# Kernel tuning notes

Hardware: AMD Instinct MI355X
Metric: run time of the kernel (lower is better)

## Reference

```python
import jax, jax.numpy as jnp
import numpy as np

D_MODEL = 1024
N_HEADS = 16
D_K = D_MODEL // N_HEADS


def setup_inputs() -> dict:
    key = jax.random.key(0)
    ks = jax.random.split(key, 11)
    B, S = 2, 2048
    scale = 1.0 / np.sqrt(D_MODEL)
    return {
        "query": jax.random.normal(ks[0], (B, S, D_MODEL), jnp.float32),
        "key": jax.random.normal(ks[1], (B, S, D_MODEL), jnp.float32),
        "value": jax.random.normal(ks[2], (B, S, D_MODEL), jnp.float32),
        "w_q": jax.random.normal(ks[3], (D_MODEL, D_MODEL), jnp.float32) * scale,
        "b_q": jnp.zeros((D_MODEL,), jnp.float32),
        "w_k": jax.random.normal(ks[4], (D_MODEL, D_MODEL), jnp.float32) * scale,
        "b_k": jnp.zeros((D_MODEL,), jnp.float32),
        "w_v": jax.random.normal(ks[5], (D_MODEL, D_MODEL), jnp.float32) * scale,
        "b_v": jnp.zeros((D_MODEL,), jnp.float32),
        "w_o": jax.random.normal(ks[6], (D_MODEL, D_MODEL), jnp.float32) * scale,
        "b_o": jnp.zeros((D_MODEL,), jnp.float32),
    }


def reference(query, key, value, w_q, b_q, w_k, b_k, w_v, b_v, w_o, b_o):
    B, S, _ = query.shape
    # Linear projections (torch Linear: x @ W.T + b), split heads -> (B, H, S, Dk)
    def proj(x, w, b):
        y = jnp.einsum('bsd,ed->bse', x, w) + b
        return y.reshape(B, -1, N_HEADS, D_K).transpose(0, 2, 1, 3)
    q = proj(query, w_q, b_q)
    k = proj(key, w_k, b_k)
    v = proj(value, w_v, b_v)
    # Scaled dot-product attention (full O(S^2) scores, faithful to source)
    scores = jnp.einsum('bhqd,bhkd->bhqk', q, k) / np.sqrt(D_K)
    attn = jax.nn.softmax(scores, axis=-1)
    out = jnp.einsum('bhqk,bhkd->bhqd', attn, v)  # (B, H, S, Dk)
    out = out.transpose(0, 2, 1, 3).reshape(B, S, D_MODEL)
    out = jnp.einsum('bsd,ed->bse', out, w_o) + b_o
    return out
```

## Files before the change

### kernel.cpp

```cpp
#include <hip/hip_runtime.h>
#include <hip/hip_bf16.h>

#define DM 1024
#define NH 16
#define DKH 64
#define BB 2
#define SS 2048
#define MM (BB*SS)
#define HKB 1024

typedef __bf16 v8bf __attribute__((ext_vector_type(8)));
typedef float  v4f  __attribute__((ext_vector_type(4)));
typedef float  v16f __attribute__((ext_vector_type(16)));

__device__ __forceinline__ unsigned short f2bf(float f) {
    union { float f; unsigned int u; } v; v.f = f;
    unsigned int u = v.u;
    unsigned int r = (u + 0x7fffu + ((u >> 16) & 1u)) >> 16;
    return (unsigned short)r;
}

__device__ __forceinline__ int cvtpk(float lo, float hi) {
    int r;
    asm("v_cvt_pk_bf16_f32 %0, %1, %2" : "=v"(r) : "v"(lo), "v"(hi));
    return r;
}

__device__ __forceinline__ void pl32swap(int& a, int& b) {
    asm("v_permlane32_swap_b32 %0, %1" : "+v"(a), "+v"(b));
}

__device__ __forceinline__ void gl16(const unsigned short* g, unsigned short* l) {
    auto gp = reinterpret_cast<const __attribute__((address_space(1))) unsigned int*>(
        reinterpret_cast<uintptr_t>(g));
    auto lp = reinterpret_cast<__attribute__((address_space(3))) unsigned int*>(
        reinterpret_cast<uintptr_t>(l));
    __builtin_amdgcn_global_load_lds(gp, lp, 16, 0, 0);
}

__global__ __launch_bounds__(256) void cvt_to_bf16(
    const float* __restrict__ xq, const float* __restrict__ xk, const float* __restrict__ xv,
    const float* __restrict__ wq, const float* __restrict__ wk, const float* __restrict__ wv,
    const float* __restrict__ wo, unsigned short* __restrict__ dst)
{
    const int y = blockIdx.y;
    const float* src;
    size_t n, off;
    if (y < 3) {
        src = (y == 0) ? xq : (y == 1) ? xk : xv;
        n = (size_t)MM * DM;
        off = (size_t)y * MM * DM;
    } else {
        src = (y == 3) ? wq : (y == 4) ? wk : (y == 5) ? wv : wo;
        n = (size_t)DM * DM;
        off = (size_t)3 * MM * DM + (size_t)(y - 3) * DM * DM;
    }
    unsigned short* d = dst + off;
    const size_t stride = (size_t)gridDim.x * blockDim.x;
    for (size_t i = (size_t)blockIdx.x * blockDim.x + threadIdx.x; i * 8 < n; i += stride) {
        float4 a = ((const float4*)src)[2 * i];
        float4 b = ((const float4*)src)[2 * i + 1];
        uint4 o;
        o.x = (unsigned)cvtpk(a.x, a.y);
        o.y = (unsigned)cvtpk(a.z, a.w);
        o.z = (unsigned)cvtpk(b.x, b.y);
        o.w = (unsigned)cvtpk(b.z, b.w);
        ((uint4*)d)[i] = o;
    }
}

__global__ __launch_bounds__(256) void proj_qkv_b(
    const unsigned short* __restrict__ xb, const unsigned short* __restrict__ wb,
    const float* __restrict__ bq, const float* __restrict__ bk, const float* __restrict__ bv,
    unsigned short* __restrict__ q_ws, unsigned short* __restrict__ k_ws,
    unsigned short* __restrict__ vt_ws)
{
    const int z = blockIdx.z;
    const unsigned short* X = xb + (size_t)z * MM * DM;
    const unsigned short* W = wb + (size_t)z * DM * DM;
    const float* bias = (z == 0) ? bq : (z == 1) ? bk : bv;

    __shared__ unsigned short lA[3][128 * 32];
    __shared__ unsigned short lB[3][128 * 32];

    const int t = threadIdx.x;
    const int lane = t & 63, w = t >> 6;
    const int wm = w >> 1, wn = w & 1;
    const int g = lane >> 4, lr = lane & 15;

    const int hid = blockIdx.y * 8 + blockIdx.x;
    const int xcd = hid & 7, slot = hid >> 3;
    const int mbase = (xcd * 4 + (slot & 3)) * 128;
    const int nbase = (slot >> 2) * 128;

    const int srow = lane >> 2;
    const int scol = (lane & 3) * 8;

    v4f acc[4][4];
#pragma unroll
    for (int i = 0; i < 4; ++i)
#pragma unroll
        for (int j = 0; j < 4; ++j)
            acc[i][j] = (v4f){0.f, 0.f, 0.f, 0.f};

    auto stage = [&](int bi, int kb) {
        gl16(X + (size_t)(mbase + w * 16 + srow) * DM + kb + scol,      &lA[bi][w * 512]);
        gl16(X + (size_t)(mbase + 64 + w * 16 + srow) * DM + kb + scol, &lA[bi][(w + 4) * 512]);
        gl16(W + (size_t)(nbase + w * 16 + srow) * DM + kb + scol,      &lB[bi][w * 512]);
        gl16(W + (size_t)(nbase + 64 + w * 16 + srow) * DM + kb + scol, &lB[bi][(w + 4) * 512]);
    };
    auto compute = [&](int bi) {
        v8bf af[4], bf4[4];
#pragma unroll
        for (int mt = 0; mt < 4; ++mt)
            af[mt] = *(const v8bf*)(&lA[bi][(wm * 64 + mt * 16 + lr) * 32 + g * 8]);
#pragma unroll
        for (int nt = 0; nt < 4; ++nt)
            bf4[nt] = *(const v8bf*)(&lB[bi][(wn * 64 + nt * 16 + lr) * 32 + g * 8]);
#pragma unroll
        for (int mt = 0; mt < 4; ++mt)
#pragma unroll
            for (int nt = 0; nt < 4; ++nt)
                acc[mt][nt] = __builtin_amdgcn_mfma_f32_16x16x32_bf16(af[mt], bf4[nt], acc[mt][nt], 0, 0, 0);
    };

    stage(0, 0);
    stage(1, 32);
    int bcur = 0;
#pragma unroll 1
    for (int ki = 0; ki < 30; ++ki) {
        int bnext = bcur + 2; if (bnext >= 3) bnext -= 3;
        stage(bnext, (ki + 2) * 32);
        asm volatile("s_waitcnt vmcnt(8)" ::: "memory");
        __builtin_amdgcn_sched_barrier(0);
        __builtin_amdgcn_s_barrier();
        __builtin_amdgcn_sched_barrier(0);
        compute(bcur);
        __builtin_amdgcn_sched_barrier(0);
        __builtin_amdgcn_s_barrier();
        bcur = (bcur == 2) ? 0 : bcur + 1;
    }
    asm volatile("s_waitcnt vmcnt(4)" ::: "memory");
    __builtin_amdgcn_sched_barrier(0);
    __builtin_amdgcn_s_barrier();
    __builtin_amdgcn_sched_barrier(0);
    compute(bcur);
    __builtin_amdgcn_sched_barrier(0);
    __builtin_amdgcn_s_barrier();
    bcur = (bcur == 2) ? 0 : bcur + 1;
    asm volatile("s_waitcnt vmcnt(0)" ::: "memory");
    __builtin_amdgcn_sched_barrier(0);
    __builtin_amdgcn_s_barrier();
    __builtin_amdgcn_sched_barrier(0);
    compute(bcur);

    const float scale = (z == 0) ? 0.18033688011112042f : 1.0f;
#pragma unroll
    for (int nt = 0; nt < 4; ++nt) {
        int e = nbase + wn * 64 + nt * 16 + lr;
        float bval = bias[e];
        int h = e >> 6, dk = e & 63;
#pragma unroll
        for (int mt = 0; mt < 4; ++mt) {
#pragma unroll
            for (int r = 0; r < 4; ++r) {
                int m = mbase + wm * 64 + mt * 16 + g * 4 + r;
                float val = (acc[mt][nt][r] + bval) * scale;
                unsigned short o = f2bf(val);
                int b = m >> 11, s = m & 2047;
                if (z == 2) {
                    vt_ws[((size_t)(b * NH + h) * DKH + dk) * SS + s] = o;
                } else {
                    unsigned short* dst = (z == 0) ? q_ws : k_ws;
                    dst[((size_t)(b * NH + h) * SS + s) * DKH + dk] = o;
                }
            }
        }
    }
}

#define KB 64
#define LDP 72
#define TILE 4608

__global__ __launch_bounds__(512, 4) void attn_kernel(
    const unsigned short* __restrict__ q_ws, const unsigned short* __restrict__ k_ws,
    const unsigned short* __restrict__ vt_ws, unsigned short* __restrict__ o_ws)
{
    __shared__ __align__(16) unsigned short lsBuf[2 * 4 * TILE];

    const int t = threadIdx.x, l = t & 63, w = t >> 6;
    const int h = l >> 5, ql = l & 31;
    const int qg = w >> 1, hf = w & 1;

    const int hid = blockIdx.x;
    const int slot = hid >> 3;
    const int bh = (hid & 7) * 4 + (slot & 3);
    const int qp = slot >> 2;
    const int q0 = qp * 128 + qg * 32;

    const unsigned short* Kb = k_ws + (size_t)bh * SS * DKH;
    const unsigned short* Vb = vt_ws + (size_t)bh * DKH * SS;

    v8bf qf[4];
#pragma unroll
    for (int c = 0; c < 4; ++c)
        qf[c] = *(const v8bf*)(q_ws + ((size_t)bh * SS + q0 + ql) * DKH + c * 16 + h * 8);

    v16f oT[2];
#pragma unroll
    for (int d = 0; d < 2; ++d)
#pragma unroll
        for (int r = 0; r < 16; ++r) oT[d][r] = 0.f;
    float l_lane = 0.f;
    const v16f z16 = {};

    const int r0s = t >> 3, c0s = (t & 7) * 8;
    uint4 k0r, k1r, v0r, v1r;

    k0r = *(const uint4*)(Kb + (size_t)(r0s) * DKH + c0s);
    v0r = *(const uint4*)(Vb + (size_t)r0s * SS + c0s);
    k1r = *(const uint4*)(Kb + (size_t)(HKB + r0s) * DKH + c0s);
    v1r = *(const uint4*)(Vb + (size_t)r0s * SS + HKB + c0s);
    {
        unsigned short* B0 = lsBuf;
        *(uint4*)&B0[0 * TILE + r0s * LDP + c0s] = k0r;
        *(uint4*)&B0[1 * TILE + r0s * LDP + c0s] = v0r;
        *(uint4*)&B0[2 * TILE + r0s * LDP + c0s] = k1r;
        *(uint4*)&B0[3 * TILE + r0s * LDP + c0s] = v1r;
    }
    k0r = *(const uint4*)(Kb + (size_t)(KB + r0s) * DKH + c0s);
    v0r = *(const uint4*)(Vb + (size_t)r0s * SS + KB + c0s);
    k1r = *(const uint4*)(Kb + (size_t)(HKB + KB + r0s) * DKH + c0s);
    v1r = *(const uint4*)(Vb + (size_t)r0s * SS + HKB + KB + c0s);
    __syncthreads();

    const int NT = 16;
    int p = 0;
    for (int tt = 0; tt < NT; ++tt) {
        unsigned short* Kp = lsBuf + p * (4 * TILE) + hf * (2 * TILE);
        unsigned short* Vp = Kp + TILE;
        if (tt + 1 < NT) {
            unsigned short* Bn = lsBuf + (p ^ 1) * (4 * TILE);
            *(uint4*)&Bn[0 * TILE + r0s * LDP + c0s] = k0r;
            *(uint4*)&Bn[1 * TILE + r0s * LDP + c0s] = v0r;
            *(uint4*)&Bn[2 * TILE + r0s * LDP + c0s] = k1r;
            *(uint4*)&Bn[3 * TILE + r0s * LDP + c0s] = v1r;
        }
        if (tt + 2 < NT) {
            int kt2 = (tt + 2) * KB;
            k0r = *(const uint4*)(Kb + (size_t)(kt2 + r0s) * DKH + c0s);
            v0r = *(const uint4*)(Vb + (size_t)r0s * SS + kt2 + c0s);
            k1r = *(const uint4*)(Kb + (size_t)(HKB + kt2 + r0s) * DKH + c0s);
            v1r = *(const uint4*)(Vb + (size_t)r0s * SS + HKB + kt2 + c0s);
        }

        v16f sT[2];
        __builtin_amdgcn_s_setprio(1);
#pragma unroll
        for (int kb = 0; kb < 2; ++kb) {
            v8bf kf = *(const v8bf*)&Kp[(kb * 32 + ql) * LDP + h * 8];
            sT[kb] = __builtin_amdgcn_mfma_f32_32x32x16_bf16(kf, qf[0], z16, 0, 0, 0);
        }
#pragma unroll
        for (int c = 1; c < 4; ++c)
#pragma unroll
            for (int kb = 0; kb < 2; ++kb) {
                v8bf kf = *(const v8bf*)&Kp[(kb * 32 + ql) * LDP + c * 16 + h * 8];
                sT[kb] = __builtin_amdgcn_mfma_f32_32x32x16_bf16(kf, qf[c], sT[kb], 0, 0, 0);
            }
        __builtin_amdgcn_s_setprio(0);

        float rs0 = 0.f, rs1 = 0.f, rs2 = 0.f, rs3 = 0.f;
#pragma unroll
        for (int kb = 0; kb < 2; ++kb)
#pragma unroll
            for (int r = 0; r < 16; r += 4) {
                float e0 = __builtin_amdgcn_exp2f(sT[kb][r + 0]);
                float e1 = __builtin_amdgcn_exp2f(sT[kb][r + 1]);
                float e2 = __builtin_amdgcn_exp2f(sT[kb][r + 2]);
                float e3 = __builtin_amdgcn_exp2f(sT[kb][r + 3]);
                sT[kb][r + 0] = e0; sT[kb][r + 1] = e1;
                sT[kb][r + 2] = e2; sT[kb][r + 3] = e3;
                rs0 += e0; rs1 += e1; rs2 += e2; rs3 += e3;
            }
        l_lane += (rs0 + rs1) + (rs2 + rs3);

        v8bf pfrag[4];
#pragma unroll
        for (int c = 0; c < 4; ++c) {
            const int cc = c & 1, kb = c >> 1;
            int A0 = cvtpk(sT[kb][8 * cc + 0], sT[kb][8 * cc + 1]);
            int A1 = cvtpk(sT[kb][8 * cc + 2], sT[kb][8 * cc + 3]);
            int B0 = cvtpk(sT[kb][8 * cc + 4], sT[kb][8 * cc + 5]);
            int B1 = cvtpk(sT[kb][8 * cc + 6], sT[kb][8 * cc + 7]);
            pl32swap(A0, B0);
            pl32swap(A1, B1);
            union { int i[4]; v8bf v; } u;
            u.i[0] = A0; u.i[1] = A1; u.i[2] = B0; u.i[3] = B1;
            pfrag[c] = u.v;
        }

        __builtin_amdgcn_s_setprio(1);
#pragma unroll
        for (int db = 0; db < 2; ++db)
#pragma unroll
            for (int c = 0; c < 4; ++c) {
                v8bf vf = *(const v8bf*)&Vp[(db * 32 + ql) * LDP + c * 16 + h * 8];
                oT[db] = __builtin_amdgcn_mfma_f32_32x32x16_bf16(vf, pfrag[c], oT[db], 0, 0, 0);
            }
        __builtin_amdgcn_s_setprio(0);

        __syncthreads();
        p ^= 1;
    }

    float lsum = l_lane + __shfl_xor(l_lane, 32);
    float* lsf = (float*)lsBuf;
    const int row = qg * 32 + ql;
#pragma unroll
    for (int db = 0; db < 2; ++db)
#pragma unroll
        for (int r = 0; r < 16; ++r) {
            int d = db * 32 + (r & 3) + 8 * (r >> 2) + 4 * h;
            lsf[(hf * 128 + row) * 65 + d] = oT[db][r];
        }
    if (h == 0) lsf[(hf * 128 + row) * 65 + 64] = lsum;
    __syncthreads();

    const int orow = t >> 2;
    const int ck = t & 3;
    const float* e0 = lsf + orow * 65;
    const float* e1 = lsf + (128 + orow) * 65;
    const float linv = 1.0f / (e0[64] + e1[64]);
    const int b = bh >> 4, hh = bh & 15;
    const int d0 = ck * 16;
    unsigned short* op = o_ws + ((size_t)b * SS + qp * 128 + orow) * DM + hh * DKH + d0;
    uint4 o0, o1;
    o0.x = (unsigned)cvtpk((e0[d0+0]+e1[d0+0])*linv,  (e0[d0+1]+e1[d0+1])*linv);
    o0.y = (unsigned)cvtpk((e0[d0+2]+e1[d0+2])*linv,  (e0[d0+3]+e1[d0+3])*linv);
    o0.z = (unsigned)cvtpk((e0[d0+4]+e1[d0+4])*linv,  (e0[d0+5]+e1[d0+5])*linv);
    o0.w = (unsigned)cvtpk((e0[d0+6]+e1[d0+6])*linv,  (e0[d0+7]+e1[d0+7])*linv);
    o1.x = (unsigned)cvtpk((e0[d0+8]+e1[d0+8])*linv,  (e0[d0+9]+e1[d0+9])*linv);
    o1.y = (unsigned)cvtpk((e0[d0+10]+e1[d0+10])*linv,(e0[d0+11]+e1[d0+11])*linv);
    o1.z = (unsigned)cvtpk((e0[d0+12]+e1[d0+12])*linv,(e0[d0+13]+e1[d0+13])*linv);
    o1.w = (unsigned)cvtpk((e0[d0+14]+e1[d0+14])*linv,(e0[d0+15]+e1[d0+15])*linv);
    *(uint4*)op = o0;
    *(uint4*)(op + 8) = o1;
}

__global__ __launch_bounds__(256) void proj_o_b(
    const unsigned short* __restrict__ A, const unsigned short* __restrict__ W,
    const float* __restrict__ bo, float* __restrict__ out)
{
    __shared__ unsigned short lA[3][128 * 32];
    __shared__ unsigned short lB[3][64 * 32];

    const int t = threadIdx.x;
    const int lane = t & 63, w = t >> 6;
    const int wm = w >> 1, wn = w & 1;
    const int g = lane >> 4, lr = lane & 15;

    const int hid = blockIdx.y * 16 + blockIdx.x;
    const int xcd = hid & 7, slot = hid >> 3;
    const int mbase = (xcd * 4 + (slot & 3)) * 128;
    const int nbase = (slot >> 2) * 64;

    const int srow = lane >> 2;
    const int scol = (lane & 3) * 8;

    v4f acc[4][2];
#pragma unroll
    for (int i = 0; i < 4; ++i)
#pragma unroll
        for (int j = 0; j < 2; ++j)
            acc[i][j] = (v4f){0.f, 0.f, 0.f, 0.f};

    auto stage = [&](int bi, int kb) {
        gl16(A + (size_t)(mbase + w * 16 + srow) * DM + kb + scol,      &lA[bi][w * 512]);
        gl16(A + (size_t)(mbase + 64 + w * 16 + srow) * DM + kb + scol, &lA[bi][(w + 4) * 512]);
        gl16(W + (size_t)(nbase + w * 16 + srow) * DM + kb + scol,      &lB[bi][w * 512]);
    };
    auto compute = [&](int bi) {
        v8bf af[4], bf4[2];
#pragma unroll
        for (int mt = 0; mt < 4; ++mt)
            af[mt] = *(const v8bf*)(&lA[bi][(wm * 64 + mt * 16 + lr) * 32 + g * 8]);
#pragma unroll
        for (int nt = 0; nt < 2; ++nt)
            bf4[nt] = *(const v8bf*)(&lB[bi][(wn * 32 + nt * 16 + lr) * 32 + g * 8]);
#pragma unroll
        for (int mt = 0; mt < 4; ++mt)
#pragma unroll
            for (int nt = 0; nt < 2; ++nt)
                acc[mt][nt] = __builtin_amdgcn_mfma_f32_16x16x32_bf16(af[mt], bf4[nt], acc[mt][nt], 0, 0, 0);
    };

    stage(0, 0);
    stage(1, 32);
    int bcur = 0;
#pragma unroll 1
    for (int ki = 0; ki < 30; ++ki) {
        int bnext = bcur + 2; if (bnext >= 3) bnext -= 3;
        stage(bnext, (ki + 2) * 32);
        asm volatile("s_waitcnt vmcnt(6)" ::: "memory");
        __builtin_amdgcn_sched_barrier(0);
        __builtin_amdgcn_s_barrier();
        __builtin_amdgcn_sched_barrier(0);
        compute(bcur);
        __builtin_amdgcn_sched_barrier(0);
        __builtin_amdgcn_s_barrier();
        bcur = (bcur == 2) ? 0 : bcur + 1;
    }
    asm volatile("s_waitcnt vmcnt(3)" ::: "memory");
    __builtin_amdgcn_sched_barrier(0);
    __builtin_amdgcn_s_barrier();
    __builtin_amdgcn_sched_barrier(0);
    compute(bcur);
    __builtin_amdgcn_sched_barrier(0);
    __builtin_amdgcn_s_barrier();
    bcur = (bcur == 2) ? 0 : bcur + 1;
    asm volatile("s_waitcnt vmcnt(0)" ::: "memory");
    __builtin_amdgcn_sched_barrier(0);
    __builtin_amdgcn_s_barrier();
    __builtin_amdgcn_sched_barrier(0);
    compute(bcur);

#pragma unroll
    for (int nt = 0; nt < 2; ++nt) {
        int e = nbase + wn * 32 + nt * 16 + lr;
        float bval = bo[e];
#pragma unroll
        for (int mt = 0; mt < 4; ++mt) {
#pragma unroll
            for (int r = 0; r < 4; ++r) {
                int m = mbase + wm * 64 + mt * 16 + g * 4 + r;
                out[(size_t)m * DM + e] = acc[mt][nt][r] + bval;
            }
        }
    }
}

extern "C" void kernel_launch(void* const* d_in, const int* in_sizes, int n_in,
                              void* d_out, int out_size, void* d_ws, size_t ws_size,
                              hipStream_t stream) {
    const float* q  = (const float*)d_in[0];
    const float* k  = (const float*)d_in[1];
    const float* v  = (const float*)d_in[2];
    const float* wq = (const float*)d_in[3];
    const float* bq = (const float*)d_in[4];
    const float* wk = (const float*)d_in[5];
    const float* bk = (const float*)d_in[6];
    const float* wv = (const float*)d_in[7];
    const float* bv = (const float*)d_in[8];
    const float* wo = (const float*)d_in[9];
    const float* bo = (const float*)d_in[10];
    float* out = (float*)d_out;

    unsigned short* ws    = (unsigned short*)d_ws;
    unsigned short* q_ws  = ws;
    unsigned short* k_ws  = q_ws + (size_t)MM * DM;
    unsigned short* vt_ws = k_ws + (size_t)MM * DM;
    unsigned short* xb    = vt_ws + (size_t)MM * DM;
    unsigned short* wb    = xb + (size_t)3 * MM * DM;
    unsigned short* o_ws  = xb;

    cvt_to_bf16<<<dim3(256, 7), 256, 0, stream>>>(q, k, v, wq, wk, wv, wo, xb);
    proj_qkv_b<<<dim3(8, 32, 3), 256, 0, stream>>>(xb, wb, bq, bk, bv, q_ws, k_ws, vt_ws);
    attn_kernel<<<dim3(512), 512, 0, stream>>>(q_ws, k_ws, vt_ws, o_ws);
    proj_o_b<<<dim3(16, 32), 256, 0, stream>>>(o_ws, wb + (size_t)3 * DM * DM, bo, out);
}
```

Measured before the change: 120.4 us.

## Fuse fp32-to-bf16 activation conversion into QKV projection GEMM loads

The activations are no longer converted to bf16 by a separate pass. The QKV projection kernel now loads fp32 activations into registers, converts them and writes them to a double-buffered LDS tile, while the weights stay on the async global-to-LDS path. The standalone conversion kernel now handles only the weights, which removes one full write and re-read of the activation tensors. The attention kernel also swaps __syncthreads for an lgkmcnt wait plus raw barrier, and interleaves exp/pack with the PV MFMAs per key block. In exchange the A tile goes through registers, which adds VGPR pressure and makes the prefetch less asynchronous.

Result: faster. 117.3 us (-2.5%).

```diff
diff --git a/kernel.cpp b/kernel.cpp
--- a/kernel.cpp
+++ b/kernel.cpp
@@ -38,24 +38,14 @@
     __builtin_amdgcn_global_load_lds(gp, lp, 16, 0, 0);
 }
 
-__global__ __launch_bounds__(256) void cvt_to_bf16(
-    const float* __restrict__ xq, const float* __restrict__ xk, const float* __restrict__ xv,
+__global__ __launch_bounds__(256) void cvt_w(
     const float* __restrict__ wq, const float* __restrict__ wk, const float* __restrict__ wv,
     const float* __restrict__ wo, unsigned short* __restrict__ dst)
 {
     const int y = blockIdx.y;
-    const float* src;
-    size_t n, off;
-    if (y < 3) {
-        src = (y == 0) ? xq : (y == 1) ? xk : xv;
-        n = (size_t)MM * DM;
-        off = (size_t)y * MM * DM;
-    } else {
-        src = (y == 3) ? wq : (y == 4) ? wk : (y == 5) ? wv : wo;
-        n = (size_t)DM * DM;
-        off = (size_t)3 * MM * DM + (size_t)(y - 3) * DM * DM;
-    }
-    unsigned short* d = dst + off;
+    const float* src = (y == 0) ? wq : (y == 1) ? wk : (y == 2) ? wv : wo;
+    unsigned short* d = dst + (size_t)y * DM * DM;
+    const size_t n = (size_t)DM * DM;
     const size_t stride = (size_t)gridDim.x * blockDim.x;
     for (size_t i = (size_t)blockIdx.x * blockDim.x + threadIdx.x; i * 8 < n; i += stride) {
         float4 a = ((const float4*)src)[2 * i];
@@ -70,17 +60,18 @@
 }
 
 __global__ __launch_bounds__(256) void proj_qkv_b(
-    const unsigned short* __restrict__ xb, const unsigned short* __restrict__ wb,
+    const float* __restrict__ Xq, const float* __restrict__ Xk, const float* __restrict__ Xv,
+    const unsigned short* __restrict__ wb,
     const float* __restrict__ bq, const float* __restrict__ bk, const float* __restrict__ bv,
     unsigned short* __restrict__ q_ws, unsigned short* __restrict__ k_ws,
     unsigned short* __restrict__ vt_ws)
 {
     const int z = blockIdx.z;
-    const unsigned short* X = xb + (size_t)z * MM * DM;
+    const float* X = (z == 0) ? Xq : (z == 1) ? Xk : Xv;
     const unsigned short* W = wb + (size_t)z * DM * DM;
     const float* bias = (z == 0) ? bq : (z == 1) ? bk : bv;
 
-    __shared__ unsigned short lA[3][128 * 32];
+    __shared__ unsigned short lA[2][128 * 32];
     __shared__ unsigned short lB[3][128 * 32];
 
     const int t = threadIdx.x;
@@ -95,6 +86,8 @@
 
     const int srow = lane >> 2;
     const int scol = (lane & 3) * 8;
+    const int arow = t >> 1;
+    const int acg  = (t & 1) * 16;
 
     v4f acc[4][4];
 #pragma unroll
@@ -103,20 +96,32 @@
         for (int j = 0; j < 4; ++j)
             acc[i][j] = (v4f){0.f, 0.f, 0.f, 0.f};
 
-    auto stage = [&](int bi, int kb) {
-        gl16(X + (size_t)(mbase + w * 16 + srow) * DM + kb + scol,      &lA[bi][w * 512]);
-        gl16(X + (size_t)(mbase + 64 + w * 16 + srow) * DM + kb + scol, &lA[bi][(w + 4) * 512]);
+    float4 ar0, ar1, ar2, ar3;
+    auto loadA = [&](int kb) {
+        const float4* p = (const float4*)(X + (size_t)(mbase + arow) * DM + kb + acg);
+        ar0 = p[0]; ar1 = p[1]; ar2 = p[2]; ar3 = p[3];
+    };
+    auto writeA = [&](int bi) {
+        uint4 o0, o1;
+        o0.x = (unsigned)cvtpk(ar0.x, ar0.y); o0.y = (unsigned)cvtpk(ar0.z, ar0.w);
+        o0.z = (unsigned)cvtpk(ar1.x, ar1.y); o0.w = (unsigned)cvtpk(ar1.z, ar1.w);
+        o1.x = (unsigned)cvtpk(ar2.x, ar2.y); o1.y = (unsigned)cvtpk(ar2.z, ar2.w);
+        o1.z = (unsigned)cvtpk(ar3.x, ar3.y); o1.w = (unsigned)cvtpk(ar3.z, ar3.w);
+        *(uint4*)&lA[bi][arow * 32 + acg]     = o0;
+        *(uint4*)&lA[bi][arow * 32 + acg + 8] = o1;
+    };
+    auto stageB = [&](int bi, int kb) {
         gl16(W + (size_t)(nbase + w * 16 + srow) * DM + kb + scol,      &lB[bi][w * 512]);
         gl16(W + (size_t)(nbase + 64 + w * 16 + srow) * DM + kb + scol, &lB[bi][(w + 4) * 512]);
     };
-    auto compute = [&](int bi) {
+    auto compute = [&](const unsigned short* A_, const unsigned short* B_) {
         v8bf af[4], bf4[4];
 #pragma unroll
         for (int mt = 0; mt < 4; ++mt)
-            af[mt] = *(const v8bf*)(&lA[bi][(wm * 64 + mt * 16 + lr) * 32 + g * 8]);
+            af[mt] = *(const v8bf*)(&A_[(wm * 64 + mt * 16 + lr) * 32 + g * 8]);
 #pragma unroll
         for (int nt = 0; nt < 4; ++nt)
-            bf4[nt] = *(const v8bf*)(&lB[bi][(wn * 64 + nt * 16 + lr) * 32 + g * 8]);
+            bf4[nt] = *(const v8bf*)(&B_[(wn * 64 + nt * 16 + lr) * 32 + g * 8]);
 #pragma unroll
         for (int mt = 0; mt < 4; ++mt)
 #pragma unroll
@@ -124,35 +129,30 @@
                 acc[mt][nt] = __builtin_amdgcn_mfma_f32_16x16x32_bf16(af[mt], bf4[nt], acc[mt][nt], 0, 0, 0);
     };
 
-    stage(0, 0);
-    stage(1, 32);
-    int bcur = 0;
+    loadA(0);
+    stageB(0, 0);
+    writeA(0);
+    loadA(32);
+    stageB(1, 32);
+
 #pragma unroll 1
-    for (int ki = 0; ki < 30; ++ki) {
-        int bnext = bcur + 2; if (bnext >= 3) bnext -= 3;
-        stage(bnext, (ki + 2) * 32);
-        asm volatile("s_waitcnt vmcnt(8)" ::: "memory");
+    for (int ki = 0; ki < 31; ++ki) {
+        writeA((ki + 1) & 1);
+        if (ki < 30) {
+            loadA((ki + 2) * 32);
+            stageB((ki + 2) % 3, (ki + 2) * 32);
+            asm volatile("s_waitcnt vmcnt(6) lgkmcnt(0)" ::: "memory");
+        } else {
+            asm volatile("s_waitcnt vmcnt(0) lgkmcnt(0)" ::: "memory");
+        }
         __builtin_amdgcn_sched_barrier(0);
         __builtin_amdgcn_s_barrier();
         __builtin_amdgcn_sched_barrier(0);
-        compute(bcur);
+        compute(lA[ki & 1], lB[ki % 3]);
         __builtin_amdgcn_sched_barrier(0);
         __builtin_amdgcn_s_barrier();
-        bcur = (bcur == 2) ? 0 : bcur + 1;
-    }
-    asm volatile("s_waitcnt vmcnt(4)" ::: "memory");
-    __builtin_amdgcn_sched_barrier(0);
-    __builtin_amdgcn_s_barrier();
-    __builtin_amdgcn_sched_barrier(0);
-    compute(bcur);
-    __builtin_amdgcn_sched_barrier(0);
-    __builtin_amdgcn_s_barrier();
-    bcur = (bcur == 2) ? 0 : bcur + 1;
-    asm volatile("s_waitcnt vmcnt(0)" ::: "memory");
-    __builtin_amdgcn_sched_barrier(0);
-    __builtin_amdgcn_s_barrier();
-    __builtin_amdgcn_sched_barrier(0);
-    compute(bcur);
+    }
+    compute(lA[31 & 1], lB[31 % 3]);
 
     const float scale = (z == 0) ? 0.18033688011112042f : 1.0f;
 #pragma unroll
@@ -233,7 +233,10 @@
     v0r = *(const uint4*)(Vb + (size_t)r0s * SS + KB + c0s);
     k1r = *(const uint4*)(Kb + (size_t)(HKB + KB + r0s) * DKH + c0s);
     v1r = *(const uint4*)(Vb + (size_t)r0s * SS + HKB + KB + c0s);
-    __syncthreads();
+    asm volatile("s_waitcnt lgkmcnt(0)" ::: "memory");
+    __builtin_amdgcn_sched_barrier(0);
+    __builtin_amdgcn_s_barrier();
+    __builtin_amdgcn_sched_barrier(0);
 
     const int NT = 16;
     int p = 0;
@@ -271,9 +274,10 @@
             }
         __builtin_amdgcn_s_setprio(0);
 
-        float rs0 = 0.f, rs1 = 0.f, rs2 = 0.f, rs3 = 0.f;
-#pragma unroll
-        for (int kb = 0; kb < 2; ++kb)
+        v8bf pfrag[4];
+#pragma unroll
+        for (int kb = 0; kb < 2; ++kb) {
+            float rs0 = 0.f, rs1 = 0.f, rs2 = 0.f, rs3 = 0.f;
 #pragma unroll
             for (int r = 0; r < 16; r += 4) {
                 float e0 = __builtin_amdgcn_exp2f(sT[kb][r + 0]);
@@ -284,34 +288,37 @@
                 sT[kb][r + 2] = e2; sT[kb][r + 3] = e3;
                 rs0 += e0; rs1 += e1; rs2 += e2; rs3 += e3;
             }
-        l_lane += (rs0 + rs1) + (rs2 + rs3);
-
-        v8bf pfrag[4];
-#pragma unroll
-        for (int c = 0; c < 4; ++c) {
-            const int cc = c & 1, kb = c >> 1;
-            int A0 = cvtpk(sT[kb][8 * cc + 0], sT[kb][8 * cc + 1]);
-            int A1 = cvtpk(sT[kb][8 * cc + 2], sT[kb][8 * cc + 3]);
-            int B0 = cvtpk(sT[kb][8 * cc + 4], sT[kb][8 * cc + 5]);
-            int B1 = cvtpk(sT[kb][8 * cc + 6], sT[kb][8 * cc + 7]);
-            pl32swap(A0, B0);
-            pl32swap(A1, B1);
-            union { int i[4]; v8bf v; } u;
-            u.i[0] = A0; u.i[1] = A1; u.i[2] = B0; u.i[3] = B1;
-            pfrag[c] = u.v;
-        }
-
-        __builtin_amdgcn_s_setprio(1);
-#pragma unroll
-        for (int db = 0; db < 2; ++db)
-#pragma unroll
-            for (int c = 0; c < 4; ++c) {
-                v8bf vf = *(const v8bf*)&Vp[(db * 32 + ql) * LDP + c * 16 + h * 8];
-                oT[db] = __builtin_amdgcn_mfma_f32_32x32x16_bf16(vf, pfrag[c], oT[db], 0, 0, 0);
+            l_lane += (rs0 + rs1) + (rs2 + rs3);
+
+#pragma unroll
+            for (int cc = 0; cc < 2; ++cc) {
+                int A0 = cvtpk(sT[kb][8 * cc + 0], sT[kb][8 * cc + 1]);
+                int A1 = cvtpk(sT[kb][8 * cc + 2], sT[kb][8 * cc + 3]);
+                int B0 = cvtpk(sT[kb][8 * cc + 4], sT[kb][8 * cc + 5]);
+                int B1 = cvtpk(sT[kb][8 * cc + 6], sT[kb][8 * cc + 7]);
+                pl32swap(A0, B0);
+                pl32swap(A1, B1);
+                union { int i[4]; v8bf v; } u;
+                u.i[0] = A0; u.i[1] = A1; u.i[2] = B0; u.i[3] = B1;
+                pfrag[kb * 2 + cc] = u.v;
             }
-        __builtin_amdgcn_s_setprio(0);
-
-        __syncthreads();
+
+            __builtin_amdgcn_s_setprio(1);
+#pragma unroll
+            for (int db = 0; db < 2; ++db)
+#pragma unroll
+                for (int cc = 0; cc < 2; ++cc) {
+                    int c = kb * 2 + cc;
+                    v8bf vf = *(const v8bf*)&Vp[(db * 32 + ql) * LDP + c * 16 + h * 8];
+                    oT[db] = __builtin_amdgcn_mfma_f32_32x32x16_bf16(vf, pfrag[c], oT[db], 0, 0, 0);
+                }
+            __builtin_amdgcn_s_setprio(0);
+        }
+
+        asm volatile("s_waitcnt lgkmcnt(0)" ::: "memory");
+        __builtin_amdgcn_sched_barrier(0);
+        __builtin_amdgcn_s_barrier();
+        __builtin_amdgcn_sched_barrier(0);
         p ^= 1;
     }
 
@@ -461,12 +468,11 @@
     unsigned short* q_ws  = ws;
     unsigned short* k_ws  = q_ws + (size_t)MM * DM;
     unsigned short* vt_ws = k_ws + (size_t)MM * DM;
-    unsigned short* xb    = vt_ws + (size_t)MM * DM;
-    unsigned short* wb    = xb + (size_t)3 * MM * DM;
-    unsigned short* o_ws  = xb;
-
-    cvt_to_bf16<<<dim3(256, 7), 256, 0, stream>>>(q, k, v, wq, wk, wv, wo, xb);
-    proj_qkv_b<<<dim3(8, 32, 3), 256, 0, stream>>>(xb, wb, bq, bk, bv, q_ws, k_ws, vt_ws);
+    unsigned short* wb    = vt_ws + (size_t)MM * DM;
+    unsigned short* o_ws  = wb + (size_t)4 * DM * DM;
+
+    cvt_w<<<dim3(64, 4), 256, 0, stream>>>(wq, wk, wv, wo, wb);
+    proj_qkv_b<<<dim3(8, 32, 3), 256, 0, stream>>>(q, k, v, wb, bq, bk, bv, q_ws, k_ws, vt_ws);
     attn_kernel<<<dim3(512), 512, 0, stream>>>(q_ws, k_ws, vt_ws, o_ws);
     proj_o_b<<<dim3(16, 32), 256, 0, stream>>>(o_ws, wb + (size_t)3 * DM * DM, bo, out);
 }
```
